# Kernel optimization log

Measured on AMD Instinct MI355X. Metric: run time of the kernel, lower is better.

Reference implementation:

```python
import jax, jax.numpy as jnp
import numpy as np

DECAY = 0.99
EPS = 1e-05
BETA = 0.25


def setup_inputs() -> dict:
    key = jax.random.key(0)
    k1, k2, k3 = jax.random.split(key, 3)
    n_embed, dim = 16384, 256
    b, h, w = 8, 32, 32
    z = jax.random.normal(k1, (b, dim, h, w), dtype=jnp.float32)
    weight = jax.random.normal(k2, (n_embed, dim), dtype=jnp.float32)
    cluster_size = jnp.zeros((n_embed,), dtype=jnp.float32)
    embed_avg = weight.copy()
    return {"z": z, "weight": weight, "cluster_size": cluster_size, "embed_avg": embed_avg}


def reference(z, weight, cluster_size, embed_avg):
    b, c, h, w = z.shape
    K, D = weight.shape
    z_perm = jnp.transpose(z, (0, 2, 3, 1))          # b h w c
    zf = z_perm.reshape(-1, D)                       # [N, D]
    # pairwise squared distances: ||z||^2 + ||e||^2 - 2 z.e
    d = (jnp.sum(zf * zf, axis=1, keepdims=True)
         + jnp.sum(weight * weight, axis=1)
         - 2.0 * jnp.einsum('nd,kd->nk', zf, weight))  # [N, K]
    idx = jnp.argmin(d, axis=1)                      # [N]
    z_q = weight[idx].reshape(b, h, w, D)
    # one-hot statistics
    encodings = jax.nn.one_hot(idx, K, dtype=z.dtype)  # [N, K]
    avg_probs = jnp.mean(encodings, axis=0)
    perplexity = jnp.exp(-jnp.sum(avg_probs * jnp.log(avg_probs + 1e-10)))
    # EMA update (training path)
    encodings_sum = jnp.sum(encodings, axis=0)                 # [K]
    embed_sum = jnp.einsum('nk,nd->kd', encodings, zf)         # [K, D]
    new_cluster_size = cluster_size * DECAY + (1.0 - DECAY) * encodings_sum
    new_embed_avg = embed_avg * DECAY + (1.0 - DECAY) * embed_sum
    n = jnp.sum(new_cluster_size)
    smoothed = (new_cluster_size + EPS) / (n + K * EPS) * n
    new_weight = new_embed_avg / smoothed[:, None]
    # commitment loss (z_q detached)
    loss = BETA * jnp.mean((jax.lax.stop_gradient(z_q) - z_perm) ** 2)
    # straight-through estimator
    z_q_st = z_perm + jax.lax.stop_gradient(z_q - z_perm)
    z_q_out = jnp.transpose(z_q_st, (0, 3, 1, 2))    # b c h w
    encoding_indices = idx.reshape(b, h, w)
    return (z_q_out, loss, perplexity, encoding_indices,
            new_weight, new_cluster_size, new_embed_avg)
```

## Files before the change

### kernel.cpp

```cpp
#include <hip/hip_runtime.h>

#define NB   8
#define DIM  256
#define HW   1024
#define NZ   8192
#define KC   16384
#define DECAYF 0.99f
#define ONEMDECAY 0.01f
#define EPSF 1e-5f
#define BETAF 0.25f
#define APHYS 512

typedef _Float16 half8 __attribute__((ext_vector_type(8)));
typedef _Float16 half4 __attribute__((ext_vector_type(4)));
typedef float floatx4 __attribute__((ext_vector_type(4)));

#define O_ZQ   0u
#define O_LOSS 2097152u
#define O_PERP 2097153u
#define O_IDX  2097154u
#define O_NW   2105346u
#define O_NCS  6299650u
#define O_NEA  6316034u

#define W_ZT     0u
#define W_WSQ    2097152u
#define W_CNT    2113536u
#define W_SCAL   2129920u
#define W_PACKED 2129924u
#define W_ACAT   2146308u
#define W_BCAT   4243460u
#define WS_FLOATS_OLD 2146308u
#define WS_FLOATS_NEW 8437764u

template <bool SPLIT>
__global__ void k_prep_fused(const float* __restrict__ z, const float* __restrict__ w,
                             const float* __restrict__ ea, float* __restrict__ zt,
                             _Float16* __restrict__ Acat, float* __restrict__ wsq,
                             _Float16* __restrict__ Bcat, float* __restrict__ out6) {
  __shared__ float tile[64][65];
  if (blockIdx.x < KC / 4) {
    int wave = threadIdx.x >> 6, lane = threadIdx.x & 63;
    int k = blockIdx.x * 4 + wave;
    float4 v = *(const float4*)&w[(size_t)k * DIM + lane * 4];
    float s = v.x * v.x + v.y * v.y + v.z * v.z + v.w * v.w;
#pragma unroll
    for (int off = 32; off; off >>= 1) s += __shfl_xor(s, off);
    if (lane == 0) wsq[k] = s;
    if (SPLIT) {
      half4 h = { (_Float16)v.x, (_Float16)v.y, (_Float16)v.z, (_Float16)v.w };
      half4 lo = { (_Float16)(v.x - (float)h.x), (_Float16)(v.y - (float)h.y),
                   (_Float16)(v.z - (float)h.z), (_Float16)(v.w - (float)h.w) };
      size_t bbase = (size_t)k * APHYS + lane * 4;
      *(half4*)&Bcat[bbase] = h;
      *(half4*)&Bcat[bbase + 256] = lo;
    }
    float4 e = *(const float4*)&ea[(size_t)k * DIM + lane * 4];
    float4 o = { DECAYF * e.x, DECAYF * e.y, DECAYF * e.z, DECAYF * e.w };
    *(float4*)&out6[(size_t)k * DIM + lane * 4] = o;
  } else {
    int flat = blockIdx.x - KC / 4;
    int hwb = (flat & 15) * 64, db = ((flat >> 4) & 3) * 64, b = flat >> 6;
    int lane = threadIdx.x & 63, sub = threadIdx.x >> 6;
#pragma unroll
    for (int i = 0; i < 16; ++i) {
      int dof = sub * 16 + i;
      tile[dof][lane] = z[((size_t)(b * DIM + db + dof)) * HW + hwb + lane];
    }
    __syncthreads();
#pragma unroll
    for (int i = 0; i < 16; ++i) {
      int hwof = sub * 16 + i;
      int n = b * HW + hwb + hwof;
      float val = tile[lane][hwof];
      zt[(size_t)n * DIM + db + lane] = val;
      if (SPLIT) {
        _Float16 h = (_Float16)val;
        _Float16 lo = (_Float16)(val - (float)h);
        size_t abase = (size_t)n * APHYS + db + lane;
        Acat[abase] = h;
        Acat[abase + 256] = lo;
      }
    }
  }
}

#define GBM 128
#define GBN 256
#define GBK 64
#define NSTEP 12

__device__ __forceinline__ void gload16(const _Float16* g, _Float16* lds) {
  __builtin_amdgcn_global_load_lds((__attribute__((address_space(1))) void*)g,
                                   (__attribute__((address_space(3))) void*)lds, 16, 0, 0);
}

#define WAITVM0   asm volatile("s_waitcnt vmcnt(0)" ::: "memory")
#define WAITLGKM0 asm volatile("s_waitcnt lgkmcnt(0)" ::: "memory")
#define BAR       __builtin_amdgcn_s_barrier()

__global__ __launch_bounds__(512, 4) void k_argmin_mfma(const _Float16* __restrict__ Acat,
                                                        const _Float16* __restrict__ Bcat,
                                                        const float* __restrict__ wsq,
                                                        unsigned long long* __restrict__ packed) {
  __shared__ __align__(16) _Float16 As[GBM * GBK];
  __shared__ __align__(16) _Float16 Bs[GBN * GBK];
  const int tid = threadIdx.x;
  const int w = tid >> 6, l = tid & 63;
  const int lr = l & 15, lc = l >> 4;
  const int wr = w >> 2, wc = w & 3;
  const int bid = (int)blockIdx.x;
  const int xcd = bid & 7, local = bid >> 3;
  const int m0 = (local >> 3) * GBM;
  const int n0 = (xcd * 8 + (local & 7)) * GBN;

  floatx4 acc[4][4];
#pragma unroll
  for (int i = 0; i < 4; ++i)
#pragma unroll
    for (int j = 0; j < 4; ++j) acc[i][j] = (floatx4){0.f, 0.f, 0.f, 0.f};

  const int srow = (l >> 3);
  const int schk = (l & 7);

#define STAGE(STEP)                                                               \
  {                                                                               \
    const int seg_ = (STEP) >> 2, ksub_ = (STEP) & 3;                             \
    const int aoff_ = (seg_ == 1 ? 256 : 0) + ksub_ * 64;                         \
    const int boff_ = (seg_ == 2 ? 256 : 0) + ksub_ * 64;                         \
    _Pragma("unroll")                                                             \
    for (int c = 0; c < 2; ++c) {                                                 \
      int row = (w * 2 + c) * 8 + srow;                                           \
      int sc_ = schk ^ (row & 7);                                                 \
      gload16(Acat + (size_t)(m0 + row) * APHYS + aoff_ + sc_ * 8,                \
              &As[(w * 2 + c) * 512]);                                            \
    }                                                                             \
    _Pragma("unroll")                                                             \
    for (int c = 0; c < 4; ++c) {                                                 \
      int row = (w * 4 + c) * 8 + srow;                                           \
      int sc_ = schk ^ (row & 7);                                                 \
      gload16(Bcat + (size_t)(n0 + row) * APHYS + boff_ + sc_ * 8,                \
              &Bs[(w * 4 + c) * 512]);                                            \
    }                                                                             \
  }

  for (int t = 0; t < NSTEP; ++t) {
    STAGE(t);
    WAITVM0;
    BAR;
#pragma unroll
    for (int kk = 0; kk < 2; ++kk) {
      half8 af[4], bf[4];
#pragma unroll
      for (int mi = 0; mi < 4; ++mi) {
        int row = wr * 64 + mi * 16 + lr;
        int ch = (kk * 4 + lc) ^ (row & 7);
        af[mi] = *(const half8*)&As[row * GBK + ch * 8];
      }
#pragma unroll
      for (int ni = 0; ni < 4; ++ni) {
        int row = wc * 64 + ni * 16 + lr;
        int ch = (kk * 4 + lc) ^ (row & 7);
        bf[ni] = *(const half8*)&Bs[row * GBK + ch * 8];
      }
#pragma unroll
      for (int mi = 0; mi < 4; ++mi)
#pragma unroll
        for (int ni = 0; ni < 4; ++ni)
          acc[mi][ni] = __builtin_amdgcn_mfma_f32_16x16x32_f16(af[mi], bf[ni], acc[mi][ni], 0, 0, 0);
    }
    WAITLGKM0;
    BAR;
  }
#undef STAGE

  unsigned long long* best = (unsigned long long*)&As[0];
  if (tid < GBM) best[tid] = ~0ull;
  __syncthreads();
  float sc4[4];
  int col4[4];
#pragma unroll
  for (int ni = 0; ni < 4; ++ni) {
    col4[ni] = n0 + wc * 64 + ni * 16 + lr;
    sc4[ni] = wsq[col4[ni]];
  }
#pragma unroll
  for (int mi = 0; mi < 4; ++mi) {
#pragma unroll
    for (int r = 0; r < 4; ++r) {
      unsigned long long bv = ~0ull;
#pragma unroll
      for (int ni = 0; ni < 4; ++ni) {
        float score = fmaf(-2.0f, acc[mi][ni][r], sc4[ni]);
        unsigned u = __float_as_uint(score);
        u ^= (unsigned)(((int)u >> 31) | 0x80000000);
        unsigned long long p = ((unsigned long long)u << 32) | (unsigned)col4[ni];
        bv = p < bv ? p : bv;
      }
#pragma unroll
      for (int off = 1; off < 16; off <<= 1) {
        unsigned long long o = __shfl_xor(bv, off);
        bv = o < bv ? o : bv;
      }
      if (lr == 0) atomicMin(&best[wr * 64 + mi * 16 + lc * 4 + r], bv);
    }
  }
  __syncthreads();
  if (tid < GBM) atomicMin(&packed[m0 + tid], best[tid]);
}

#define TM 128
#define TN 128
#define DK 32
#define PADL 33
__global__ __launch_bounds__(256) void k_argmin_fp32(const float* __restrict__ zt,
                                                     const float* __restrict__ w,
                                                     const float* __restrict__ wsq,
                                                     unsigned long long* __restrict__ packed) {
  __shared__ float As[TM * PADL];
  __shared__ float Ws[TN * PADL];
  __shared__ unsigned long long best[TM];
  const int tid = threadIdx.x;
  const int k0 = blockIdx.x * TN, m0 = blockIdx.y * TM;
  if (tid < TM) best[tid] = ~0ull;
  const int tx = tid & 15, ty = tid >> 4;
  const int mrow = tid & 127;
  const int q = (tid >> 7) * 16;

  float acc[8][8];
#pragma unroll
  for (int i = 0; i < 8; ++i)
#pragma unroll
    for (int j = 0; j < 8; ++j) acc[i][j] = 0.0f;

  for (int dbase = 0; dbase < DIM; dbase += DK) {
    __syncthreads();
    const float* za = &zt[(size_t)(m0 + mrow) * DIM + dbase + q];
    const float* wa = &w[(size_t)(k0 + mrow) * DIM + dbase + q];
    float4 a0 = *(const float4*)(za + 0), a1 = *(const float4*)(za + 4);
    float4 a2 = *(const float4*)(za + 8), a3 = *(const float4*)(za + 12);
    float4 b0 = *(const float4*)(wa + 0), b1 = *(const float4*)(wa + 4);
    float4 b2 = *(const float4*)(wa + 8), b3 = *(const float4*)(wa + 12);
    float* Ap = &As[mrow * PADL + q];
    float* Wp = &Ws[mrow * PADL + q];
    Ap[0] = a0.x; Ap[1] = a0.y; Ap[2] = a0.z; Ap[3] = a0.w;
    Ap[4] = a1.x; Ap[5] = a1.y; Ap[6] = a1.z; Ap[7] = a1.w;
    Ap[8] = a2.x; Ap[9] = a2.y; Ap[10] = a2.z; Ap[11] = a2.w;
    Ap[12] = a3.x; Ap[13] = a3.y; Ap[14] = a3.z; Ap[15] = a3.w;
    Wp[0] = b0.x; Wp[1] = b0.y; Wp[2] = b0.z; Wp[3] = b0.w;
    Wp[4] = b1.x; Wp[5] = b1.y; Wp[6] = b1.z; Wp[7] = b1.w;
    Wp[8] = b2.x; Wp[9] = b2.y; Wp[10] = b2.z; Wp[11] = b2.w;
    Wp[12] = b3.x; Wp[13] = b3.y; Wp[14] = b3.z; Wp[15] = b3.w;
    __syncthreads();
#pragma unroll
    for (int d = 0; d < DK; ++d) {
      float a[8], b[8];
#pragma unroll
      for (int i = 0; i < 4; ++i) {
        a[i]     = As[(ty * 4 + i) * PADL + d];
        a[4 + i] = As[(64 + ty * 4 + i) * PADL + d];
        b[i]     = Ws[(tx * 4 + i) * PADL + d];
        b[4 + i] = Ws[(64 + tx * 4 + i) * PADL + d];
      }
#pragma unroll
      for (int i = 0; i < 8; ++i)
#pragma unroll
        for (int j = 0; j < 8; ++j) acc[i][j] = fmaf(a[i], b[j], acc[i][j]);
    }
  }

  float sc[8];
  int cols[8];
#pragma unroll
  for (int j = 0; j < 8; ++j) {
    int c = (j < 4) ? tx * 4 + j : 64 + tx * 4 + (j - 4);
    cols[j] = k0 + c;
    sc[j] = wsq[cols[j]];
  }
#pragma unroll
  for (int i = 0; i < 8; ++i) {
    int r = (i < 4) ? ty * 4 + i : 64 + ty * 4 + (i - 4);
    unsigned long long bv = ~0ull;
#pragma unroll
    for (int j = 0; j < 8; ++j) {
      float score = fmaf(-2.0f, acc[i][j], sc[j]);
      unsigned u = __float_as_uint(score);
      u ^= (unsigned)(((int)u >> 31) | 0x80000000);
      unsigned long long p = ((unsigned long long)u << 32) | (unsigned)cols[j];
      bv = p < bv ? p : bv;
    }
    atomicMin(&best[r], bv);
  }
  __syncthreads();
  if (tid < TM) atomicMin(&packed[m0 + tid], best[tid]);
}

__global__ __launch_bounds__(256) void k_scatter(float* __restrict__ zt,
                                                 const float* __restrict__ w,
                                                 const unsigned long long* __restrict__ packed,
                                                 float* __restrict__ emb_out,
                                                 float* __restrict__ loss_sum,
                                                 float* __restrict__ out3,
                                                 float* __restrict__ counts) {
  int n = blockIdx.x, d = threadIdx.x;
  int k = (int)(packed[n] & 0xFFFFFFFFull) & (KC - 1);
  if (d == 0) {
    out3[n] = (float)k;
    atomicAdd(&counts[k], 1.0f);
  }
  float zv = zt[(size_t)n * DIM + d];
  float wv = w[(size_t)k * DIM + d];
  float diff = wv - zv;
  zt[(size_t)n * DIM + d] = zv + diff;
  atomicAdd(&emb_out[(size_t)k * DIM + d], ONEMDECAY * zv);
  float v = diff * diff;
#pragma unroll
  for (int off = 32; off; off >>= 1) v += __shfl_down(v, off);
  __shared__ float red[4];
  if ((threadIdx.x & 63) == 0) red[threadIdx.x >> 6] = v;
  __syncthreads();
  if (threadIdx.x == 0) atomicAdd(loss_sum, red[0] + red[1] + red[2] + red[3]);
}

__global__ void k_cs(const float* __restrict__ cs, const float* __restrict__ counts,
                     float* __restrict__ out5, float* __restrict__ scal) {
  int k = blockIdx.x * 256 + threadIdx.x;
  float c = counts[k];
  float ncs = cs[k] * DECAYF + ONEMDECAY * c;
  out5[k] = ncs;
  float p = c * (1.0f / (float)NZ);
  float t = p * logf(p + 1e-10f);
#pragma unroll
  for (int off = 32; off; off >>= 1) {
    ncs += __shfl_down(ncs, off);
    t += __shfl_down(t, off);
  }
  __shared__ float r1[4], r2[4];
  if ((threadIdx.x & 63) == 0) { r1[threadIdx.x >> 6] = ncs; r2[threadIdx.x >> 6] = t; }
  __syncthreads();
  if (threadIdx.x == 0) {
    atomicAdd(&scal[1], r1[0] + r1[1] + r1[2] + r1[3]);
    atomicAdd(&scal[2], r2[0] + r2[1] + r2[2] + r2[3]);
  }
}

__global__ void k_final_fused(const float* __restrict__ emb_out, const float* __restrict__ out5,
                              const float* __restrict__ scal, const float* __restrict__ zt,
                              float* __restrict__ out4, float* __restrict__ out1,
                              float* __restrict__ out2, float* __restrict__ out0) {
  __shared__ float tile[64][65];
  if (blockIdx.x < (KC * DIM) / 256) {
    size_t i = (size_t)blockIdx.x * 256 + threadIdx.x;
    float n = scal[1];
    int k = (int)(i >> 8);
    float ncs = out5[k];
    float smoothed = (ncs + EPSF) / (n + (float)KC * EPSF) * n;
    out4[i] = emb_out[i] / smoothed;
    if (i == 0) {
      out1[0] = BETAF * scal[0] / (float)(NZ * DIM);
      out2[0] = expf(-scal[2]);
    }
  } else {
    int flat = blockIdx.x - (KC * DIM) / 256;
    int hwb = (flat & 15) * 64, db = ((flat >> 4) & 3) * 64, b = flat >> 6;
    int lane = threadIdx.x & 63, sub = threadIdx.x >> 6;
#pragma unroll
    for (int i = 0; i < 16; ++i) {
      int hwof = sub * 16 + i;
      tile[hwof][lane] = zt[((size_t)(b * HW + hwb + hwof)) * DIM + db + lane];
    }
    __syncthreads();
#pragma unroll
    for (int i = 0; i < 16; ++i) {
      int dof = sub * 16 + i;
      out0[((size_t)(b * DIM + db + dof)) * HW + hwb + lane] = tile[lane][dof];
    }
  }
}

extern "C" void kernel_launch(void* const* d_in, const int* in_sizes, int n_in,
                              void* d_out, int out_size, void* d_ws, size_t ws_size,
                              hipStream_t stream) {
  const float* z  = (const float*)d_in[0];
  const float* w  = (const float*)d_in[1];
  const float* cs = (const float*)d_in[2];
  const float* ea = (const float*)d_in[3];
  float* out = (float*)d_out;
  float* ws  = (float*)d_ws;

  if (ws_size < (size_t)WS_FLOATS_OLD * sizeof(float)) return;
  const bool use_mfma = ws_size >= (size_t)WS_FLOATS_NEW * sizeof(float);

  float* zt      = ws + W_ZT;
  float* wsq     = ws + W_WSQ;
  float* counts  = ws + W_CNT;
  float* scal    = ws + W_SCAL;
  unsigned long long* packed = (unsigned long long*)(ws + W_PACKED);
  _Float16* Acat = (_Float16*)(ws + W_ACAT);
  _Float16* Bcat = (_Float16*)(ws + W_BCAT);

  float* out0 = out + O_ZQ;
  float* out1 = out + O_LOSS;
  float* out2 = out + O_PERP;
  float* out3 = out + O_IDX;
  float* out4 = out + O_NW;
  float* out5 = out + O_NCS;
  float* out6 = out + O_NEA;

  hipMemsetAsync(counts, 0, (16384 + 4) * sizeof(float), stream);
  hipMemsetAsync(packed, 0xFF, (size_t)NZ * sizeof(unsigned long long), stream);

  if (use_mfma) {
    k_prep_fused<true><<<KC / 4 + 512, 256, 0, stream>>>(z, w, ea, zt, Acat, wsq, Bcat, out6);
    k_argmin_mfma<<<(KC / GBN) * (NZ / GBM), 512, 0, stream>>>(Acat, Bcat, wsq, packed);
  } else {
    k_prep_fused<false><<<KC / 4 + 512, 256, 0, stream>>>(z, w, ea, zt, Acat, wsq, Bcat, out6);
    k_argmin_fp32<<<dim3(KC / TN, NZ / TM), 256, 0, stream>>>(zt, w, wsq, packed);
  }
  k_scatter<<<NZ, 256, 0, stream>>>(zt, w, packed, out6, scal, out3, counts);
  k_cs<<<KC / 256, 256, 0, stream>>>(cs, counts, out5, scal);
  k_final_fused<<<(KC * DIM) / 256 + 512, 256, 0, stream>>>(out6, out5, scal, zt,
                                                            out4, out1, out2, out0);
}
```

Measured before the change: 390.2 us.

## Fold cluster-size kernel into prep/final, vectorize scatter and final update

```diff
diff --git a/kernel.cpp b/kernel.cpp
--- a/kernel.cpp
+++ b/kernel.cpp
@@ -35,9 +35,10 @@
 
 template <bool SPLIT>
 __global__ void k_prep_fused(const float* __restrict__ z, const float* __restrict__ w,
-                             const float* __restrict__ ea, float* __restrict__ zt,
-                             _Float16* __restrict__ Acat, float* __restrict__ wsq,
-                             _Float16* __restrict__ Bcat, float* __restrict__ out6) {
+                             const float* __restrict__ ea, const float* __restrict__ cs,
+                             float* __restrict__ zt, _Float16* __restrict__ Acat,
+                             float* __restrict__ wsq, _Float16* __restrict__ Bcat,
+                             float* __restrict__ out6, float* __restrict__ scal) {
   __shared__ float tile[64][65];
   if (blockIdx.x < KC / 4) {
     int wave = threadIdx.x >> 6, lane = threadIdx.x & 63;
@@ -58,7 +59,7 @@
     float4 e = *(const float4*)&ea[(size_t)k * DIM + lane * 4];
     float4 o = { DECAYF * e.x, DECAYF * e.y, DECAYF * e.z, DECAYF * e.w };
     *(float4*)&out6[(size_t)k * DIM + lane * 4] = o;
-  } else {
+  } else if (blockIdx.x < KC / 4 + 512) {
     int flat = blockIdx.x - KC / 4;
     int hwb = (flat & 15) * 64, db = ((flat >> 4) & 3) * 64, b = flat >> 6;
     int lane = threadIdx.x & 63, sub = threadIdx.x >> 6;
@@ -82,6 +83,15 @@
         Acat[abase + 256] = lo;
       }
     }
+  } else {
+    int idx = (blockIdx.x - (KC / 4 + 512)) * 256 + threadIdx.x;
+    float v = cs[idx];
+#pragma unroll
+    for (int off = 32; off; off >>= 1) v += __shfl_xor(v, off);
+    __shared__ float r[4];
+    if ((threadIdx.x & 63) == 0) r[threadIdx.x >> 6] = v;
+    __syncthreads();
+    if (threadIdx.x == 0) atomicAdd(&scal[3], r[0] + r[1] + r[2] + r[3]);
   }
 }
 
@@ -302,66 +312,68 @@
                                                  float* __restrict__ loss_sum,
                                                  float* __restrict__ out3,
                                                  float* __restrict__ counts) {
-  int n = blockIdx.x, d = threadIdx.x;
-  int k = (int)(packed[n] & 0xFFFFFFFFull) & (KC - 1);
-  if (d == 0) {
+  const int r = threadIdx.x >> 6, lane = threadIdx.x & 63;
+  const int n = blockIdx.x * 4 + r;
+  const int k = (int)(packed[n] & 0xFFFFFFFFull) & (KC - 1);
+  if (lane == 0) {
     out3[n] = (float)k;
     atomicAdd(&counts[k], 1.0f);
   }
-  float zv = zt[(size_t)n * DIM + d];
-  float wv = w[(size_t)k * DIM + d];
-  float diff = wv - zv;
-  zt[(size_t)n * DIM + d] = zv + diff;
-  atomicAdd(&emb_out[(size_t)k * DIM + d], ONEMDECAY * zv);
-  float v = diff * diff;
+  const size_t zb = (size_t)n * DIM + lane * 4;
+  const size_t wb = (size_t)k * DIM + lane * 4;
+  float4 zv = *(const float4*)&zt[zb];
+  float4 wv = *(const float4*)&w[wb];
+  float4 df = { wv.x - zv.x, wv.y - zv.y, wv.z - zv.z, wv.w - zv.w };
+  float4 st = { zv.x + df.x, zv.y + df.y, zv.z + df.z, zv.w + df.w };
+  *(float4*)&zt[zb] = st;
+  atomicAdd(&emb_out[wb + 0], ONEMDECAY * zv.x);
+  atomicAdd(&emb_out[wb + 1], ONEMDECAY * zv.y);
+  atomicAdd(&emb_out[wb + 2], ONEMDECAY * zv.z);
+  atomicAdd(&emb_out[wb + 3], ONEMDECAY * zv.w);
+  float v = df.x * df.x + df.y * df.y + df.z * df.z + df.w * df.w;
 #pragma unroll
   for (int off = 32; off; off >>= 1) v += __shfl_down(v, off);
   __shared__ float red[4];
-  if ((threadIdx.x & 63) == 0) red[threadIdx.x >> 6] = v;
+  if (lane == 0) red[r] = v;
   __syncthreads();
   if (threadIdx.x == 0) atomicAdd(loss_sum, red[0] + red[1] + red[2] + red[3]);
 }
 
-__global__ void k_cs(const float* __restrict__ cs, const float* __restrict__ counts,
-                     float* __restrict__ out5, float* __restrict__ scal) {
-  int k = blockIdx.x * 256 + threadIdx.x;
-  float c = counts[k];
-  float ncs = cs[k] * DECAYF + ONEMDECAY * c;
-  out5[k] = ncs;
-  float p = c * (1.0f / (float)NZ);
-  float t = p * logf(p + 1e-10f);
-#pragma unroll
-  for (int off = 32; off; off >>= 1) {
-    ncs += __shfl_down(ncs, off);
-    t += __shfl_down(t, off);
-  }
-  __shared__ float r1[4], r2[4];
-  if ((threadIdx.x & 63) == 0) { r1[threadIdx.x >> 6] = ncs; r2[threadIdx.x >> 6] = t; }
-  __syncthreads();
-  if (threadIdx.x == 0) {
-    atomicAdd(&scal[1], r1[0] + r1[1] + r1[2] + r1[3]);
-    atomicAdd(&scal[2], r2[0] + r2[1] + r2[2] + r2[3]);
-  }
-}
-
-__global__ void k_final_fused(const float* __restrict__ emb_out, const float* __restrict__ out5,
-                              const float* __restrict__ scal, const float* __restrict__ zt,
-                              float* __restrict__ out4, float* __restrict__ out1,
+__global__ void k_final_fused(const float* __restrict__ emb_out, const float* __restrict__ cs,
+                              const float* __restrict__ counts, const float* __restrict__ scal,
+                              const float* __restrict__ zt, float* __restrict__ out4,
+                              float* __restrict__ out5, float* __restrict__ out1,
                               float* __restrict__ out2, float* __restrict__ out0) {
   __shared__ float tile[64][65];
-  if (blockIdx.x < (KC * DIM) / 256) {
-    size_t i = (size_t)blockIdx.x * 256 + threadIdx.x;
-    float n = scal[1];
-    int k = (int)(i >> 8);
-    float ncs = out5[k];
-    float smoothed = (ncs + EPSF) / (n + (float)KC * EPSF) * n;
-    out4[i] = emb_out[i] / smoothed;
-    if (i == 0) {
+  if (blockIdx.x < (KC * DIM) / 1024) {
+    int i4 = blockIdx.x * 256 + threadIdx.x;
+    int k = i4 >> 6;
+    float c = counts[k];
+    float ncs = cs[k] * DECAYF + ONEMDECAY * c;
+    if ((i4 & 63) == 0) out5[k] = ncs;
+    float nsum = DECAYF * scal[3] + ONEMDECAY * (float)NZ;
+    float smoothed = (ncs + EPSF) / (nsum + (float)KC * EPSF) * nsum;
+    float inv = 1.0f / smoothed;
+    float4 e = *(const float4*)&emb_out[(size_t)i4 * 4];
+    float4 o = { e.x * inv, e.y * inv, e.z * inv, e.w * inv };
+    *(float4*)&out4[(size_t)i4 * 4] = o;
+  } else if (blockIdx.x == (KC * DIM) / 1024) {
+    float t = 0.0f;
+    for (int i = threadIdx.x; i < KC; i += 256) {
+      float p = counts[i] * (1.0f / (float)NZ);
+      t += p * logf(p + 1e-10f);
+    }
+#pragma unroll
+    for (int off = 32; off; off >>= 1) t += __shfl_down(t, off);
+    __shared__ float r2[4];
+    if ((threadIdx.x & 63) == 0) r2[threadIdx.x >> 6] = t;
+    __syncthreads();
+    if (threadIdx.x == 0) {
+      out2[0] = expf(-(r2[0] + r2[1] + r2[2] + r2[3]));
       out1[0] = BETAF * scal[0] / (float)(NZ * DIM);
-      out2[0] = expf(-scal[2]);
     }
   } else {
-    int flat = blockIdx.x - (KC * DIM) / 256;
+    int flat = blockIdx.x - ((KC * DIM) / 1024 + 1);
     int hwb = (flat & 15) * 64, db = ((flat >> 4) & 3) * 64, b = flat >> 6;
     int lane = threadIdx.x & 63, sub = threadIdx.x >> 6;
 #pragma unroll
@@ -411,14 +423,15 @@
   hipMemsetAsync(packed, 0xFF, (size_t)NZ * sizeof(unsigned long long), stream);
 
   if (use_mfma) {
-    k_prep_fused<true><<<KC / 4 + 512, 256, 0, stream>>>(z, w, ea, zt, Acat, wsq, Bcat, out6);
+    k_prep_fused<true><<<KC / 4 + 512 + 64, 256, 0, stream>>>(z, w, ea, cs, zt, Acat,
+                                                              wsq, Bcat, out6, scal);
     k_argmin_mfma<<<(KC / GBN) * (NZ / GBM), 512, 0, stream>>>(Acat, Bcat, wsq, packed);
   } else {
-    k_prep_fused<false><<<KC / 4 + 512, 256, 0, stream>>>(z, w, ea, zt, Acat, wsq, Bcat, out6);
+    k_prep_fused<false><<<KC / 4 + 512 + 64, 256, 0, stream>>>(z, w, ea, cs, zt, Acat,
+                                                               wsq, Bcat, out6, scal);
     k_argmin_fp32<<<dim3(KC / TN, NZ / TM), 256, 0, stream>>>(zt, w, wsq, packed);
   }
-  k_scatter<<<NZ, 256, 0, stream>>>(zt, w, packed, out6, scal, out3, counts);
-  k_cs<<<KC / 256, 256, 0, stream>>>(cs, counts, out5, scal);
-  k_final_fused<<<(KC * DIM) / 256 + 512, 256, 0, stream>>>(out6, out5, scal, zt,
-                                                            out4, out1, out2, out0);
-}
+  k_scatter<<<NZ / 4, 256, 0, stream>>>(zt, w, packed, out6, scal, out3, counts);
+  k_final_fused<<<(KC * DIM) / 1024 + 1 + 512, 256, 0, stream>>>(out6, cs, counts, scal, zt,
+                                                                 out4, out5, out1, out2, out0);
+}
```

Result: faster. 340.9 us (-12.6%).
